# Performance work log

Measured on AMD Instinct MI355X. Metric: run time of the kernel, lower is better.

Reference implementation:

```python
import jax, jax.numpy as jnp
import numpy as np

WS = 8       # window size
NH = 6       # num heads
SHIFT = 4    # ws//2 since index=1 (shifted)
EPS = 1e-6


def _rel_pos_index(ws):
    coords = np.stack(np.meshgrid(np.arange(ws), np.arange(ws), indexing='ij'))  # (2,ws,ws)
    cf = coords.reshape(2, -1)
    rel = (cf[:, :, None] - cf[:, None, :]).transpose(1, 2, 0)  # (N,N,2)
    rel[..., 0] += ws - 1
    rel[..., 1] += ws - 1
    rel[..., 0] *= 2 * ws - 1
    return rel.sum(-1)  # (N,N) int


def _attn_mask(H, W, ws, shift):
    img = np.zeros((H, W))
    slices = (slice(0, -ws), slice(-ws, -shift), slice(-shift, None))
    cnt = 0
    for h in slices:
        for w in slices:
            img[h, w] = cnt
            cnt += 1
    mw = img.reshape(H // ws, ws, W // ws, ws).transpose(0, 2, 1, 3).reshape(-1, ws * ws)
    am = mw[:, None, :] - mw[:, :, None]  # (nW,N,N): unsqueeze(1) - unsqueeze(2)
    return np.where(am != 0, -100.0, 0.0).astype(np.float32)


def layernorm2d(x, w, b):
    mu = x.mean(1, keepdims=True)
    var = ((x - mu) ** 2).mean(1, keepdims=True)
    y = (x - mu) / jnp.sqrt(var + EPS)
    return w[None, :, None, None] * y + b[None, :, None, None]


def window_partition(x, ws):
    B, C, H, W = x.shape
    x = x.reshape(B, C, H // ws, ws, W // ws, ws)
    return x.transpose(0, 2, 4, 3, 5, 1).reshape(-1, ws * ws, C)


def window_reverse(win, ws, H, W):
    B = win.shape[0] // ((H // ws) * (W // ws))
    x = win.reshape(B, H // ws, W // ws, ws, ws, -1)
    return x.transpose(0, 5, 1, 3, 2, 4).reshape(B, -1, H, W)


def shifted_window_attn(x, qkv_w, qkv_b, proj_w, proj_b, rpb_table):
    B, C, H, W = x.shape
    N = WS * WS
    hd = C // NH
    scale = hd ** -0.5
    # faithful to original: raw reshape BCHW->BHWC (reinterpretation), roll, reshape back
    x = jnp.roll(x.reshape(B, H, W, C), (-SHIFT, -SHIFT), (1, 2)).reshape(B, C, H, W)
    win = window_partition(x, WS)  # (B_, N, C)
    B_ = win.shape[0]
    qkv = (win @ qkv_w + qkv_b).reshape(B_, N, 3, NH, hd).transpose(2, 0, 3, 1, 4)
    q, k, v = qkv[0] * scale, qkv[1], qkv[2]
    attn = jnp.einsum('bhnd,bhmd->bhnm', q, k)  # (B_,NH,N,N)
    rpi = _rel_pos_index(WS)
    bias = rpb_table[rpi.reshape(-1)].reshape(N, N, NH).transpose(2, 0, 1)
    attn = attn + bias[None]
    mask = jnp.asarray(_attn_mask(H, W, WS, SHIFT))  # (nW,N,N)
    nW = mask.shape[0]
    attn = attn.reshape(B_ // nW, nW, NH, N, N) + mask[None, :, None]
    attn = jax.nn.softmax(attn.reshape(B_, NH, N, N), axis=-1)
    out = jnp.einsum('bhnm,bhmd->bhnd', attn, v).transpose(0, 2, 1, 3).reshape(B_, N, C)
    out = out @ proj_w + proj_b
    return window_reverse(out, WS, H, W)


def channel_attention(y, ca_w, ca_b):
    gap = y.mean((2, 3))  # (B,C)
    s = jnp.einsum('bc,oc->bo', gap, ca_w) + ca_b  # 1x1 conv on pooled feature
    return s[:, :, None, None]


def mlp(y, fc1_w, fc1_b, fc2_w, fc2_b):
    B, C, H, W = y.shape
    t = y.transpose(0, 2, 3, 1)  # (B,H,W,C)
    t = jax.nn.gelu(t @ fc1_w + fc1_b, approximate=False)
    t = t @ fc2_w + fc2_b
    return t.transpose(0, 3, 1, 2)


def setup_inputs() -> dict:
    key = jax.random.key(0)
    ks = jax.random.split(key, 8)
    C, H, W, B = 192, 256, 256, 2
    hid = 2 * C
    sc = 0.02
    return {
        'x': jax.random.normal(ks[0], (B, C, H, W), jnp.float32),
        'norm1_w': jnp.ones((C,), jnp.float32),
        'norm1_b': jnp.zeros((C,), jnp.float32),
        'qkv_w': jax.random.normal(ks[1], (C, 3 * C), jnp.float32) * sc,
        'qkv_b': jnp.zeros((3 * C,), jnp.float32),
        'proj_w': jax.random.normal(ks[2], (C, C), jnp.float32) * sc,
        'proj_b': jnp.zeros((C,), jnp.float32),
        'rpb_table': jax.random.normal(ks[3], ((2 * WS - 1) ** 2, NH), jnp.float32) * sc,
        'ca_w': jax.random.normal(ks[4], (C, C), jnp.float32) * sc,
        'ca_b': jnp.zeros((C,), jnp.float32),
        'norm2_w': jnp.ones((C,), jnp.float32),
        'norm2_b': jnp.zeros((C,), jnp.float32),
        'fc1_w': jax.random.normal(ks[5], (C, hid), jnp.float32) * sc,
        'fc1_b': jnp.zeros((hid,), jnp.float32),
        'fc2_w': jax.random.normal(ks[6], (hid, C), jnp.float32) * sc,
        'fc2_b': jnp.zeros((C,), jnp.float32),
    }


def reference(x, norm1_w, norm1_b, qkv_w, qkv_b, proj_w, proj_b, rpb_table,
              ca_w, ca_b, norm2_w, norm2_b, fc1_w, fc1_b, fc2_w, fc2_b):
    y = layernorm2d(x, norm1_w, norm1_b)
    y = shifted_window_attn(y, qkv_w, qkv_b, proj_w, proj_b, rpb_table)
    y = y * channel_attention(y, ca_w, ca_b)
    x = x + y
    y2 = mlp(layernorm2d(x, norm2_w, norm2_b), fc1_w, fc1_b, fc2_w, fc2_b)
    return x + y2
```

## Files before the change

kernel.cpp:

```cpp
#include <hip/hip_runtime.h>
#include <hip/hip_bf16.h>
#include <stdint.h>

#define C_   192
#define H_   256
#define W_   256
#define HW_  65536
#define CHW  12582912
#define NH_  6
#define HID_ 384

typedef __attribute__((ext_vector_type(8))) __bf16 bf16x8;
typedef __attribute__((ext_vector_type(4))) float  fx4;

__device__ __forceinline__ uint16_t f2bf(float f) {
  uint32_t u = __builtin_bit_cast(uint32_t, f);
  u += 0x7fffu + ((u >> 16) & 1u);
  return (uint16_t)(u >> 16);
}
__device__ __forceinline__ float bf2f(uint16_t h) {
  uint32_t u = ((uint32_t)h) << 16;
  return __builtin_bit_cast(float, u);
}
__device__ __forceinline__ uint32_t pk2(float a, float b) {
  return (uint32_t)f2bf(a) | ((uint32_t)f2bf(b) << 16);
}
__device__ __forceinline__ bf16x8 ld8(const uint16_t* p) {
  uint4 v = *reinterpret_cast<const uint4*>(p);
  return __builtin_bit_cast(bf16x8, v);
}
__device__ __forceinline__ fx4 mfma16(bf16x8 a, bf16x8 b, fx4 c) {
  return __builtin_amdgcn_mfma_f32_16x16x32_bf16(a, b, c, 0, 0, 0);
}

__global__ __launch_bounds__(256) void prep_kernel(
    const float* __restrict__ qkv_w, const float* __restrict__ proj_w,
    const float* __restrict__ fc1_w, const float* __restrict__ fc2_w,
    const float* __restrict__ rpb,
    uint16_t* __restrict__ qkv_wt, uint16_t* __restrict__ proj_wt,
    uint16_t* __restrict__ fc1_wt, uint16_t* __restrict__ fc2_wt,
    float* __restrict__ rpbb) {
  int tid = blockIdx.x * 256 + threadIdx.x;
  if (tid < 576 * 192) {
    int f = tid / 192, k = tid % 192;
    qkv_wt[tid] = f2bf(qkv_w[k * 576 + f]);
  }
  int t1 = tid - 576 * 192;
  if (t1 >= 0 && t1 < 192 * 192) {
    int f = t1 / 192, k = t1 % 192;
    proj_wt[t1] = f2bf(proj_w[k * 192 + f]);
  }
  int t2 = t1 - 192 * 192;
  if (t2 >= 0 && t2 < 384 * 192) {
    int f = t2 / 192, k = t2 % 192;
    fc1_wt[t2] = f2bf(fc1_w[k * 384 + f]);
  }
  int t3 = t2 - 384 * 192;
  if (t3 >= 0 && t3 < 192 * 384) {
    int f = t3 / 384, k = t3 % 384;
    fc2_wt[t3] = f2bf(fc2_w[k * 192 + f]);
  }
  int t4 = t3 - 192 * 384;
  if (t4 >= 0 && t4 < 6 * 64 * 64) {
    int h = t4 / 4096, nm = t4 % 4096, n = nm / 64, m = nm % 64;
    int yn = n >> 3, xn = n & 7, ym = m >> 3, xm = m & 7;
    int idx = (yn - ym + 7) * 15 + (xn - xm + 7);
    rpbb[t4] = rpb[idx * NH_ + h];
  }
}

__global__ __launch_bounds__(256) void ln1_stats(const float* __restrict__ x,
                                                 float* __restrict__ mu,
                                                 float* __restrict__ rsig) {
  int t = blockIdx.x * 256 + threadIdx.x;
  int b = t >> 16, hw = t & 65535;
  const float* xp = x + (size_t)b * CHW + hw;
  float s = 0.f, sq = 0.f;
#pragma unroll 8
  for (int c = 0; c < C_; c++) {
    float v = xp[(size_t)c * HW_];
    s += v; sq += v * v;
  }
  float m = s * (1.0f / C_);
  float var = sq * (1.0f / C_) - m * m;
  mu[t] = m;
  rsig[t] = rsqrtf(var + 1e-6f);
}

__global__ __launch_bounds__(256) void ln1_apply_kernel(
    const float* __restrict__ x, const float* __restrict__ mu, const float* __restrict__ rsig,
    const float* __restrict__ n1w, const float* __restrict__ n1b,
    uint16_t* __restrict__ y_tok) {
  __shared__ __attribute__((aligned(16))) uint16_t tile[192 * 66];
  int wg = blockIdx.x;
  int b = wg >> 10, hw0 = (wg & 1023) << 6;
  int t = threadIdx.x;
  const float* xb = x + (size_t)b * CHW;
  const float* mub = mu + b * HW_;
  const float* rsb = rsig + b * HW_;
#pragma unroll 4
  for (int it = 0; it < 48; it++) {
    int id = it * 256 + t;
    int ca = id >> 6, pp = id & 63;
    int g = ca * 65536 + hw0 + pp;
    int h2 = g / 49152;
    int r = g - h2 * 49152;
    int w2 = r / 192;
    int c2 = r - w2 * 192;
    int f = ((h2 + 4) & 255) * 49152 + ((w2 + 4) & 255) * 192 + c2;
    int cnat = f >> 16;
    int hwn = f & 65535;
    float v = (xb[f] - mub[hwn]) * rsb[hwn] * n1w[cnat] + n1b[cnat];
    tile[ca * 66 + pp] = f2bf(v);
  }
  __syncthreads();
  uint16_t* yb = y_tok + ((size_t)(b * HW_ + hw0)) * C_;
#pragma unroll 4
  for (int it = 0; it < 48; it++) {
    int id = it * 256 + t;
    int pp = id / 192, ca = id - pp * 192;
    yb[id] = tile[ca * 66 + pp];
  }
}

__global__ __launch_bounds__(256, 2) void attn_kernel(
    const uint16_t* __restrict__ y_tok, const uint16_t* __restrict__ qkv_wt,
    const float* __restrict__ qkv_b, const uint16_t* __restrict__ proj_wt,
    const float* __restrict__ proj_b, const float* __restrict__ rpbb,
    uint16_t* __restrict__ y_attn, float* __restrict__ part) {
  __shared__ __attribute__((aligned(16))) uint16_t Qs[64 * 200];
  __shared__ __attribute__((aligned(16))) uint16_t Ks[64 * 200];
  __shared__ __attribute__((aligned(16))) uint16_t VT[32 * 72];
  __shared__ __attribute__((aligned(16))) uint16_t Ps[64 * 72];
  const int wg = blockIdx.x;
  const int b = wg >> 10, wid = wg & 1023;
  const int wh = wid >> 5, ww = wid & 31;
  const int t = threadIdx.x;
  const int w = t >> 6, l = t & 63;
  const int lane16 = l & 15, quad = l >> 4;
  const int trow = w * 16 + quad * 4;

  bf16x8 afr[4][6];
#pragma unroll
  for (int m = 0; m < 4; m++) {
    const int tok = m * 16 + lane16;
    const uint16_t* ap = y_tok +
        ((size_t)(b * HW_ + (wh * 8 + (tok >> 3)) * W_ + ww * 8 + (tok & 7))) * C_ + quad * 8;
#pragma unroll
    for (int k = 0; k < 6; k++) afr[m][k] = ld8(ap + k * 32);
  }

  const float scale = 0.17677669529663687f;
  uint32_t vpack[3][4][2];

#pragma unroll
  for (int j = 0; j < 3; j++) {
    const int nt = w + 4 * j;
    const uint16_t* bp = qkv_wt + (nt * 16 + lane16) * C_ + quad * 8;
    bf16x8 bfr[6];
#pragma unroll
    for (int k = 0; k < 6; k++) bfr[k] = ld8(bp + k * 32);
    fx4 acc[4];
#pragma unroll
    for (int m = 0; m < 4; m++) acc[m] = fx4{0.f, 0.f, 0.f, 0.f};
#pragma unroll
    for (int k = 0; k < 6; k++)
#pragma unroll
      for (int m = 0; m < 4; m++) acc[m] = mfma16(afr[m][k], bfr[k], acc[m]);
    const int f = nt * 16 + lane16;
    const float bias = qkv_b[f];
#pragma unroll
    for (int m = 0; m < 4; m++)
#pragma unroll
      for (int r = 0; r < 4; r++)
        Qs[(m * 16 + quad * 4 + r) * 200 + f] = f2bf((acc[m][r] + bias) * scale);
  }
#pragma unroll
  for (int j = 3; j < 6; j++) {
    const int nt = w + 4 * j;
    const uint16_t* bp = qkv_wt + (nt * 16 + lane16) * C_ + quad * 8;
    bf16x8 bfr[6];
#pragma unroll
    for (int k = 0; k < 6; k++) bfr[k] = ld8(bp + k * 32);
    fx4 acc[4];
#pragma unroll
    for (int m = 0; m < 4; m++) acc[m] = fx4{0.f, 0.f, 0.f, 0.f};
#pragma unroll
    for (int k = 0; k < 6; k++)
#pragma unroll
      for (int m = 0; m < 4; m++) acc[m] = mfma16(afr[m][k], bfr[k], acc[m]);
    const int f = nt * 16 + lane16;
    const float bias = qkv_b[f];
#pragma unroll
    for (int m = 0; m < 4; m++)
#pragma unroll
      for (int r = 0; r < 4; r++)
        Ks[(m * 16 + quad * 4 + r) * 200 + (f - 192)] = f2bf(acc[m][r] + bias);
  }
#pragma unroll
  for (int j = 6; j < 9; j++) {
    const int nt = w + 4 * j;
    const uint16_t* bp = qkv_wt + (nt * 16 + lane16) * C_ + quad * 8;
    bf16x8 bfr[6];
#pragma unroll
    for (int k = 0; k < 6; k++) bfr[k] = ld8(bp + k * 32);
    fx4 acc[4];
#pragma unroll
    for (int m = 0; m < 4; m++) acc[m] = fx4{0.f, 0.f, 0.f, 0.f};
#pragma unroll
    for (int k = 0; k < 6; k++)
#pragma unroll
      for (int m = 0; m < 4; m++) acc[m] = mfma16(afr[m][k], bfr[k], acc[m]);
    const float bias = qkv_b[nt * 16 + lane16];
    const int jv = j - 6;
#pragma unroll
    for (int m = 0; m < 4; m++) {
      vpack[jv][m][0] = pk2(acc[m][0] + bias, acc[m][1] + bias);
      vpack[jv][m][1] = pk2(acc[m][2] + bias, acc[m][3] + bias);
    }
  }

  const bool whe = (wh == 31), wwe = (ww == 31);

  for (int h = 0; h < 6; h++) {
    __syncthreads();
    {
      const int vt0 = 2 * h, vt1 = 2 * h + 1;
      if (w == (vt0 & 3)) {
        const int jv = vt0 >> 2;
#pragma unroll
        for (int m = 0; m < 4; m++) {
          uint2 vv; vv.x = vpack[jv][m][0]; vv.y = vpack[jv][m][1];
          *reinterpret_cast<uint2*>(&VT[lane16 * 72 + m * 16 + quad * 4]) = vv;
        }
      }
      if (w == (vt1 & 3)) {
        const int jv = vt1 >> 2;
#pragma unroll
        for (int m = 0; m < 4; m++) {
          uint2 vv; vv.x = vpack[jv][m][0]; vv.y = vpack[jv][m][1];
          *reinterpret_cast<uint2*>(&VT[(16 + lane16) * 72 + m * 16 + quad * 4]) = vv;
        }
      }
    }
    __syncthreads();

    const bf16x8 qa = ld8(&Qs[(w * 16 + lane16) * 200 + h * 32 + quad * 8]);
    fx4 sacc[4];
#pragma unroll
    for (int nt = 0; nt < 4; nt++) {
      const bf16x8 kb = ld8(&Ks[(nt * 16 + lane16) * 200 + h * 32 + quad * 8]);
      fx4 z = {0.f, 0.f, 0.f, 0.f};
      sacc[nt] = mfma16(qa, kb, z);
    }
    const float* rb = rpbb + h * 4096;
#pragma unroll
    for (int nt = 0; nt < 4; nt++) {
      const int ct = nt * 16 + lane16;
      const bool rbc = whe && ((ct >> 3) >= 4);
      const bool cbc = wwe && ((ct & 7) >= 4);
#pragma unroll
      for (int r = 0; r < 4; r++) {
        const int rt = trow + r;
        const bool rbr = whe && ((rt >> 3) >= 4);
        const bool cbr = wwe && ((rt & 7) >= 4);
        float v = sacc[nt][r] + rb[rt * 64 + ct];
        if (rbr != rbc || cbr != cbc) v -= 100.f;
        sacc[nt][r] = v;
      }
    }
    float sm[4];
#pragma unroll
    for (int r = 0; r < 4; r++) {
      float m = fmaxf(fmaxf(sacc[0][r], sacc[1][r]), fmaxf(sacc[2][r], sacc[3][r]));
      m = fmaxf(m, __shfl_xor(m, 1));
      m = fmaxf(m, __shfl_xor(m, 2));
      m = fmaxf(m, __shfl_xor(m, 4));
      m = fmaxf(m, __shfl_xor(m, 8));
      float s0 = 0.f;
#pragma unroll
      for (int nt = 0; nt < 4; nt++) {
        float e = exp2f((sacc[nt][r] - m) * 1.4426950408889634f);
        sacc[nt][r] = e; s0 += e;
      }
      s0 += __shfl_xor(s0, 1);
      s0 += __shfl_xor(s0, 2);
      s0 += __shfl_xor(s0, 4);
      s0 += __shfl_xor(s0, 8);
      sm[r] = s0;
    }
#pragma unroll
    for (int nt = 0; nt < 4; nt++)
#pragma unroll
      for (int r = 0; r < 4; r++)
        Ps[(trow + r) * 72 + nt * 16 + lane16] = f2bf(sacc[nt][r]);
    fx4 o0 = {0.f, 0.f, 0.f, 0.f}, o1 = {0.f, 0.f, 0.f, 0.f};
#pragma unroll
    for (int ks2 = 0; ks2 < 2; ks2++) {
      const bf16x8 pa = ld8(&Ps[(w * 16 + lane16) * 72 + ks2 * 32 + quad * 8]);
      const bf16x8 v0 = ld8(&VT[(lane16) * 72 + ks2 * 32 + quad * 8]);
      const bf16x8 v1 = ld8(&VT[(16 + lane16) * 72 + ks2 * 32 + quad * 8]);
      o0 = mfma16(pa, v0, o0);
      o1 = mfma16(pa, v1, o1);
    }
#pragma unroll
    for (int r = 0; r < 4; r++) {
      const float inv = 1.0f / sm[r];
      Qs[(trow + r) * 200 + h * 32 + lane16] = f2bf(o0[r] * inv);
      Qs[(trow + r) * 200 + h * 32 + 16 + lane16] = f2bf(o1[r] * inv);
    }
  }
  __syncthreads();

  bf16x8 ofr[4][6];
#pragma unroll
  for (int m = 0; m < 4; m++)
#pragma unroll
    for (int k = 0; k < 6; k++)
      ofr[m][k] = ld8(&Qs[(m * 16 + lane16) * 200 + k * 32 + quad * 8]);

  uint16_t* yb = y_attn + (size_t)b * HW_ * C_;
  uint32_t obase[4][4];
#pragma unroll
  for (int m = 0; m < 4; m++)
#pragma unroll
    for (int r = 0; r < 4; r++) {
      const int tok = m * 16 + quad * 4 + r;
      obase[m][r] = (uint32_t)(((wh * 8 + (tok >> 3)) * W_ + ww * 8 + (tok & 7)) * C_);
    }
#pragma unroll
  for (int j = 0; j < 3; j++) {
    const int nt = w + 4 * j;
    const uint16_t* bp = proj_wt + (nt * 16 + lane16) * C_ + quad * 8;
    bf16x8 bfr[6];
#pragma unroll
    for (int k = 0; k < 6; k++) bfr[k] = ld8(bp + k * 32);
    fx4 acc[4];
#pragma unroll
    for (int m = 0; m < 4; m++) acc[m] = fx4{0.f, 0.f, 0.f, 0.f};
#pragma unroll
    for (int k = 0; k < 6; k++)
#pragma unroll
      for (int m = 0; m < 4; m++) acc[m] = mfma16(ofr[m][k], bfr[k], acc[m]);
    const float pb = proj_b[nt * 16 + lane16];
    float cs = 0.f;
#pragma unroll
    for (int m = 0; m < 4; m++)
#pragma unroll
      for (int r = 0; r < 4; r++) {
        const float v = acc[m][r] + pb;
        yb[obase[m][r] + nt * 16 + lane16] = f2bf(v);
        cs += v;
      }
    cs += __shfl_xor(cs, 16);
    cs += __shfl_xor(cs, 32);
    if (l < 16) part[(size_t)wg * 192 + nt * 16 + lane16] = cs;
  }
}

__global__ __launch_bounds__(768) void ca_s_kernel(const float* __restrict__ part,
                                                   const float* __restrict__ ca_w,
                                                   const float* __restrict__ ca_b,
                                                   float* __restrict__ sbuf) {
  int b = blockIdx.x;
  int t = threadIdx.x;
  __shared__ float red[768];
  __shared__ float gap[192];
  int g = t / 192, c = t - g * 192;
  float s = 0.f;
#pragma unroll 8
  for (int i = g; i < 1024; i += 4) s += part[((size_t)b * 1024 + i) * 192 + c];
  red[t] = s;
  __syncthreads();
  if (t < 192)
    gap[t] = (red[t] + red[t + 192] + red[t + 384] + red[t + 576]) * (1.0f / 65536.0f);
  __syncthreads();
  if (t < 192) {
    float acc = ca_b[t];
#pragma unroll 8
    for (int c2 = 0; c2 < 192; c2++) acc += gap[c2] * ca_w[t * 192 + c2];
    sbuf[b * 192 + t] = acc;
  }
}

__global__ __launch_bounds__(256, 3) void resid_ln2(
    const float* __restrict__ x, const uint16_t* __restrict__ y_attn,
    const float* __restrict__ sbuf, const float* __restrict__ n2w,
    const float* __restrict__ n2b, uint16_t* __restrict__ t2) {
  __shared__ __attribute__((aligned(16))) float tile[192 * 66];
  __shared__ float red[512];
  __shared__ float mus[128];
  int wg = blockIdx.x;
  int b = wg >> 10, hw0 = (wg & 1023) << 6;
  int t = threadIdx.x;
#pragma unroll 4
  for (int it = 0; it < 48; it++) {
    int id = it * 256 + t;
    int c = id >> 6, p = id & 63;
    tile[c * 66 + p] = x[(size_t)b * CHW + (size_t)c * HW_ + hw0 + p];
  }
  __syncthreads();
#pragma unroll 4
  for (int it = 0; it < 48; it++) {
    int id = it * 256 + t;
    int p = id / 192, c = id - p * 192;
    float y = bf2f(y_attn[((size_t)(b * HW_ + hw0 + p)) * C_ + c]);
    tile[c * 66 + p] += sbuf[b * 192 + c] * y;
  }
  __syncthreads();
  {
    int p = t & 63, g = t >> 6;
    float s = 0.f, sq = 0.f;
    for (int c = g * 48; c < g * 48 + 48; c++) {
      float v = tile[c * 66 + p];
      s += v; sq += v * v;
    }
    red[g * 64 + p] = s;
    red[256 + g * 64 + p] = sq;
  }
  __syncthreads();
  if (t < 64) {
    float ss = red[t] + red[64 + t] + red[128 + t] + red[192 + t];
    float qq = red[256 + t] + red[320 + t] + red[384 + t] + red[448 + t];
    float m = ss * (1.0f / C_);
    float var = qq * (1.0f / C_) - m * m;
    mus[t] = m;
    mus[64 + t] = rsqrtf(var + 1e-6f);
  }
  __syncthreads();
#pragma unroll 4
  for (int it = 0; it < 48; it++) {
    int id = it * 256 + t;
    int p = id / 192, c = id - p * 192;
    float v = (tile[c * 66 + p] - mus[p]) * mus[64 + p] * n2w[c] + n2b[c];
    t2[((size_t)(b * HW_ + hw0 + p)) * C_ + c] = f2bf(v);
  }
}

__global__ __launch_bounds__(256, 3) void mlp_kernel(
    const uint16_t* __restrict__ t2, const uint16_t* __restrict__ fc1_wt,
    const float* __restrict__ fc1_b, const uint16_t* __restrict__ fc2_wt,
    const float* __restrict__ fc2_b, const float* __restrict__ x,
    const uint16_t* __restrict__ y_attn, const float* __restrict__ sbuf,
    float* __restrict__ out) {
  __shared__ __attribute__((aligned(16))) char smem[192 * 66 * 4];
  __shared__ float sarr[192];
  uint16_t* hbuf = (uint16_t*)smem;
  float* ftile = (float*)smem;
  int wg = blockIdx.x;
  int b = wg >> 10, hw0 = (wg & 1023) << 6;
  int t = threadIdx.x;
  int w = t >> 6, l = t & 63;
  int lane16 = l & 15, quad = l >> 4;
  if (t < 192) sarr[t] = sbuf[b * 192 + t];

  bf16x8 afr[4][6];
  const uint16_t* ab = t2 + ((size_t)(b * HW_ + hw0)) * C_;
#pragma unroll
  for (int m = 0; m < 4; m++) {
    const uint16_t* ap = ab + (m * 16 + lane16) * C_ + quad * 8;
#pragma unroll
    for (int k = 0; k < 6; k++) afr[m][k] = ld8(ap + k * 32);
  }

#pragma unroll
  for (int j = 0; j < 6; j++) {
    const int nt = w + 4 * j;
    const uint16_t* bp = fc1_wt + (nt * 16 + lane16) * C_ + quad * 8;
    bf16x8 bfr[6];
#pragma unroll
    for (int k = 0; k < 6; k++) bfr[k] = ld8(bp + k * 32);
    fx4 acc[4];
#pragma unroll
    for (int m = 0; m < 4; m++) acc[m] = fx4{0.f, 0.f, 0.f, 0.f};
#pragma unroll
    for (int k = 0; k < 6; k++)
#pragma unroll
      for (int m = 0; m < 4; m++) acc[m] = mfma16(afr[m][k], bfr[k], acc[m]);
    const float bias = fc1_b[nt * 16 + lane16];
#pragma unroll
    for (int m = 0; m < 4; m++)
#pragma unroll
      for (int r = 0; r < 4; r++) {
        float v = acc[m][r] + bias;
        float ge = 0.5f * v * (1.0f + erff(v * 0.7071067811865476f));
        hbuf[(m * 16 + quad * 4 + r) * 392 + nt * 16 + lane16] = f2bf(ge);
      }
  }
  __syncthreads();

  fx4 acc2[3][4];
#pragma unroll
  for (int j = 0; j < 3; j++)
#pragma unroll
    for (int m = 0; m < 4; m++) acc2[j][m] = fx4{0.f, 0.f, 0.f, 0.f};
#pragma unroll
  for (int kc = 0; kc < 4; kc++) {
    bf16x8 ha[4][3];
#pragma unroll
    for (int m = 0; m < 4; m++)
#pragma unroll
      for (int kk = 0; kk < 3; kk++)
        ha[m][kk] = ld8(&hbuf[(m * 16 + lane16) * 392 + kc * 96 + kk * 32 + quad * 8]);
#pragma unroll
    for (int j = 0; j < 3; j++) {
      const int nt = w + 4 * j;
      const uint16_t* bp = fc2_wt + (nt * 16 + lane16) * HID_ + kc * 96 + quad * 8;
#pragma unroll
      for (int kk = 0; kk < 3; kk++) {
        const bf16x8 bb = ld8(bp + kk * 32);
#pragma unroll
        for (int m = 0; m < 4; m++) acc2[j][m] = mfma16(ha[m][kk], bb, acc2[j][m]);
      }
    }
  }
  __syncthreads();

#pragma unroll
  for (int j = 0; j < 3; j++) {
    const int nt = w + 4 * j;
    const float bias = fc2_b[nt * 16 + lane16];
#pragma unroll
    for (int m = 0; m < 4; m++) {
      float* fp = &ftile[(nt * 16 + lane16) * 66 + m * 16 + quad * 4];
      float2 a = {acc2[j][m][0] + bias, acc2[j][m][1] + bias};
      float2 b2 = {acc2[j][m][2] + bias, acc2[j][m][3] + bias};
      *reinterpret_cast<float2*>(fp) = a;
      *reinterpret_cast<float2*>(fp + 2) = b2;
    }
  }
  __syncthreads();
#pragma unroll 4
  for (int it = 0; it < 48; it++) {
    int id = it * 256 + t;
    int p = id / 192, c = id - p * 192;
    float y = bf2f(y_attn[((size_t)(b * HW_ + hw0 + p)) * C_ + c]);
    ftile[c * 66 + p] += sarr[c] * y;
  }
  __syncthreads();
#pragma unroll 4
  for (int it = 0; it < 48; it++) {
    int id = it * 256 + t;
    int c = id >> 6, p = id & 63;
    size_t gi = (size_t)b * CHW + (size_t)c * HW_ + hw0 + p;
    out[gi] = x[gi] + ftile[c * 66 + p];
  }
}

extern "C" void kernel_launch(void* const* d_in, const int* in_sizes, int n_in,
                              void* d_out, int out_size, void* d_ws, size_t ws_size,
                              hipStream_t stream) {
  const float* x      = (const float*)d_in[0];
  const float* n1w    = (const float*)d_in[1];
  const float* n1b    = (const float*)d_in[2];
  const float* qkv_w  = (const float*)d_in[3];
  const float* qkv_b  = (const float*)d_in[4];
  const float* proj_w = (const float*)d_in[5];
  const float* proj_b = (const float*)d_in[6];
  const float* rpb    = (const float*)d_in[7];
  const float* ca_w   = (const float*)d_in[8];
  const float* ca_b   = (const float*)d_in[9];
  const float* n2w    = (const float*)d_in[10];
  const float* n2b    = (const float*)d_in[11];
  const float* fc1_w  = (const float*)d_in[12];
  const float* fc1_b  = (const float*)d_in[13];
  const float* fc2_w  = (const float*)d_in[14];
  const float* fc2_b  = (const float*)d_in[15];
  float* out = (float*)d_out;

  char* ws = (char*)d_ws;
  uint16_t* y_tok   = (uint16_t*)(ws + 0);
  uint16_t* y_attn  = (uint16_t*)(ws + 50331648);
  uint16_t* t2      = y_tok;
  float*    mu      = (float*)   (ws + 100663296);
  float*    rsig    = (float*)   (ws + 101187584);
  uint16_t* qkv_wt  = (uint16_t*)(ws + 101711872);
  uint16_t* proj_wt = (uint16_t*)(ws + 101933056);
  uint16_t* fc1_wt  = (uint16_t*)(ws + 102006784);
  uint16_t* fc2_wt  = (uint16_t*)(ws + 102154240);
  float*    rpbb    = (float*)   (ws + 102301696);
  float*    part    = (float*)   (ws + 102400000);
  float*    sbuf    = (float*)   (ws + 103972864);

  hipLaunchKernelGGL(prep_kernel, dim3(1248), dim3(256), 0, stream,
                     qkv_w, proj_w, fc1_w, fc2_w, rpb, qkv_wt, proj_wt, fc1_wt, fc2_wt, rpbb);
  hipLaunchKernelGGL(ln1_stats, dim3(512), dim3(256), 0, stream, x, mu, rsig);
  hipLaunchKernelGGL(ln1_apply_kernel, dim3(2048), dim3(256), 0, stream,
                     x, mu, rsig, n1w, n1b, y_tok);
  hipLaunchKernelGGL(attn_kernel, dim3(2048), dim3(256), 0, stream,
                     y_tok, qkv_wt, qkv_b, proj_wt, proj_b, rpbb, y_attn, part);
  hipLaunchKernelGGL(ca_s_kernel, dim3(2), dim3(768), 0, stream, part, ca_w, ca_b, sbuf);
  hipLaunchKernelGGL(resid_ln2, dim3(2048), dim3(256), 0, stream,
                     x, y_attn, sbuf, n2w, n2b, t2);
  hipLaunchKernelGGL(mlp_kernel, dim3(2048), dim3(256), 0, stream,
                     t2, fc1_wt, fc1_b, fc2_wt, fc2_b, x, y_attn, sbuf, out);
}
```

Before: 577.5 us.

## Shrink MLP tile to 32 tokens, use tanh GELU, split channel-attention reduction

The MLP kernel now handles 32 tokens per block instead of 64, launches twice as many blocks and raises the occupancy hint from 3 to 4. Each wave computes one 16-row M tile across a wider N range, which lowers register and LDS use per block. The erf GELU is replaced with an exp2/rcp tanh approximation, and the epilogue uses vectorized bf16x8 and float2 loads and stores. The channel-attention global pooling, previously done by 2 blocks, is split into a 128-block partial-sum kernel plus a small final kernel. In exchange, weight fragments are reused across fewer tokens, and the tanh GELU slightly changes numerics.

```diff
diff --git a/kernel.cpp b/kernel.cpp
--- a/kernel.cpp
+++ b/kernel.cpp
@@ -11,6 +11,7 @@
 #define HID_ 384
 
 typedef __attribute__((ext_vector_type(8))) __bf16 bf16x8;
+typedef __attribute__((ext_vector_type(8))) uint16_t u16x8;
 typedef __attribute__((ext_vector_type(4))) float  fx4;
 
 __device__ __forceinline__ uint16_t f2bf(float f) {
@@ -31,6 +32,14 @@
 }
 __device__ __forceinline__ fx4 mfma16(bf16x8 a, bf16x8 b, fx4 c) {
   return __builtin_amdgcn_mfma_f32_16x16x32_bf16(a, b, c, 0, 0, 0);
+}
+__device__ __forceinline__ float gelu_f(float v) {
+  float c2 = v * v;
+  float u = __builtin_fmaf(c2, 0.044715f, 1.0f) * v;
+  float e = exp2f(u * 2.3022084f);
+  float th = 1.0f - 2.0f * __builtin_amdgcn_rcpf(1.0f + e);
+  float hv = 0.5f * v;
+  return __builtin_fmaf(hv, th, hv);
 }
 
 __global__ __launch_bounds__(256) void prep_kernel(
@@ -358,29 +367,34 @@
   }
 }
 
-__global__ __launch_bounds__(768) void ca_s_kernel(const float* __restrict__ part,
-                                                   const float* __restrict__ ca_w,
-                                                   const float* __restrict__ ca_b,
-                                                   float* __restrict__ sbuf) {
+__global__ __launch_bounds__(192) void ca_gap(const float* __restrict__ part,
+                                              float* __restrict__ gpart) {
+  int blk = blockIdx.x;
+  int b = blk >> 6, ch = blk & 63;
+  int c = threadIdx.x;
+  float s = 0.f;
+#pragma unroll
+  for (int i = 0; i < 16; i++)
+    s += part[((size_t)b * 1024 + ch * 16 + i) * 192 + c];
+  gpart[blk * 192 + c] = s;
+}
+
+__global__ __launch_bounds__(192) void ca_s2(const float* __restrict__ gpart,
+                                             const float* __restrict__ ca_w,
+                                             const float* __restrict__ ca_b,
+                                             float* __restrict__ sbuf) {
   int b = blockIdx.x;
   int t = threadIdx.x;
-  __shared__ float red[768];
   __shared__ float gap[192];
-  int g = t / 192, c = t - g * 192;
   float s = 0.f;
 #pragma unroll 8
-  for (int i = g; i < 1024; i += 4) s += part[((size_t)b * 1024 + i) * 192 + c];
-  red[t] = s;
-  __syncthreads();
-  if (t < 192)
-    gap[t] = (red[t] + red[t + 192] + red[t + 384] + red[t + 576]) * (1.0f / 65536.0f);
-  __syncthreads();
-  if (t < 192) {
-    float acc = ca_b[t];
+  for (int i = 0; i < 64; i++) s += gpart[(b * 64 + i) * 192 + t];
+  gap[t] = s * (1.0f / 65536.0f);
+  __syncthreads();
+  float acc = ca_b[t];
 #pragma unroll 8
-    for (int c2 = 0; c2 < 192; c2++) acc += gap[c2] * ca_w[t * 192 + c2];
-    sbuf[b * 192 + t] = acc;
-  }
+  for (int c2 = 0; c2 < 192; c2++) acc += gap[c2] * ca_w[t * 192 + c2];
+  sbuf[b * 192 + t] = acc;
 }
 
 __global__ __launch_bounds__(256, 3) void resid_ln2(
@@ -437,113 +451,106 @@
   }
 }
 
-__global__ __launch_bounds__(256, 3) void mlp_kernel(
+__global__ __launch_bounds__(256, 4) void mlp_kernel(
     const uint16_t* __restrict__ t2, const uint16_t* __restrict__ fc1_wt,
     const float* __restrict__ fc1_b, const uint16_t* __restrict__ fc2_wt,
     const float* __restrict__ fc2_b, const float* __restrict__ x,
     const uint16_t* __restrict__ y_attn, const float* __restrict__ sbuf,
     float* __restrict__ out) {
-  __shared__ __attribute__((aligned(16))) char smem[192 * 66 * 4];
+  __shared__ __attribute__((aligned(16))) char smem[192 * 34 * 4];
   __shared__ float sarr[192];
   uint16_t* hbuf = (uint16_t*)smem;
   float* ftile = (float*)smem;
   int wg = blockIdx.x;
-  int b = wg >> 10, hw0 = (wg & 1023) << 6;
+  int b = wg >> 11, hw0 = (wg & 2047) << 5;
   int t = threadIdx.x;
   int w = t >> 6, l = t & 63;
   int lane16 = l & 15, quad = l >> 4;
+  const int m1 = w & 1, ng = w >> 1;
   if (t < 192) sarr[t] = sbuf[b * 192 + t];
 
-  bf16x8 afr[4][6];
-  const uint16_t* ab = t2 + ((size_t)(b * HW_ + hw0)) * C_;
-#pragma unroll
-  for (int m = 0; m < 4; m++) {
-    const uint16_t* ap = ab + (m * 16 + lane16) * C_ + quad * 8;
-#pragma unroll
-    for (int k = 0; k < 6; k++) afr[m][k] = ld8(ap + k * 32);
-  }
-
-#pragma unroll
-  for (int j = 0; j < 6; j++) {
-    const int nt = w + 4 * j;
+  bf16x8 afr[6];
+  {
+    const uint16_t* ap = t2 + ((size_t)(b * HW_ + hw0 + m1 * 16 + lane16)) * C_ + quad * 8;
+#pragma unroll
+    for (int k = 0; k < 6; k++) afr[k] = ld8(ap + k * 32);
+  }
+
+#pragma unroll 4
+  for (int j = 0; j < 12; j++) {
+    const int nt = ng * 12 + j;
     const uint16_t* bp = fc1_wt + (nt * 16 + lane16) * C_ + quad * 8;
     bf16x8 bfr[6];
 #pragma unroll
     for (int k = 0; k < 6; k++) bfr[k] = ld8(bp + k * 32);
-    fx4 acc[4];
-#pragma unroll
-    for (int m = 0; m < 4; m++) acc[m] = fx4{0.f, 0.f, 0.f, 0.f};
-#pragma unroll
-    for (int k = 0; k < 6; k++)
-#pragma unroll
-      for (int m = 0; m < 4; m++) acc[m] = mfma16(afr[m][k], bfr[k], acc[m]);
+    fx4 acc = {0.f, 0.f, 0.f, 0.f};
+#pragma unroll
+    for (int k = 0; k < 6; k++) acc = mfma16(afr[k], bfr[k], acc);
     const float bias = fc1_b[nt * 16 + lane16];
 #pragma unroll
-    for (int m = 0; m < 4; m++)
-#pragma unroll
-      for (int r = 0; r < 4; r++) {
-        float v = acc[m][r] + bias;
-        float ge = 0.5f * v * (1.0f + erff(v * 0.7071067811865476f));
-        hbuf[(m * 16 + quad * 4 + r) * 392 + nt * 16 + lane16] = f2bf(ge);
+    for (int r = 0; r < 4; r++) {
+      float ge = gelu_f(acc[r] + bias);
+      hbuf[(m1 * 16 + quad * 4 + r) * 392 + nt * 16 + lane16] = f2bf(ge);
+    }
+  }
+  __syncthreads();
+
+  fx4 acc2[6];
+#pragma unroll
+  for (int j = 0; j < 6; j++) acc2[j] = fx4{0.f, 0.f, 0.f, 0.f};
+#pragma unroll
+  for (int kc = 0; kc < 4; kc++) {
+#pragma unroll
+    for (int kk = 0; kk < 3; kk++) {
+      const bf16x8 ha = ld8(&hbuf[(m1 * 16 + lane16) * 392 + kc * 96 + kk * 32 + quad * 8]);
+#pragma unroll
+      for (int j = 0; j < 6; j++) {
+        const int nt2 = ng * 6 + j;
+        const bf16x8 bb = ld8(fc2_wt + (nt2 * 16 + lane16) * HID_ + kc * 96 + kk * 32 + quad * 8);
+        acc2[j] = mfma16(ha, bb, acc2[j]);
       }
-  }
-  __syncthreads();
-
-  fx4 acc2[3][4];
-#pragma unroll
-  for (int j = 0; j < 3; j++)
-#pragma unroll
-    for (int m = 0; m < 4; m++) acc2[j][m] = fx4{0.f, 0.f, 0.f, 0.f};
-#pragma unroll
-  for (int kc = 0; kc < 4; kc++) {
-    bf16x8 ha[4][3];
-#pragma unroll
-    for (int m = 0; m < 4; m++)
-#pragma unroll
-      for (int kk = 0; kk < 3; kk++)
-        ha[m][kk] = ld8(&hbuf[(m * 16 + lane16) * 392 + kc * 96 + kk * 32 + quad * 8]);
-#pragma unroll
-    for (int j = 0; j < 3; j++) {
-      const int nt = w + 4 * j;
-      const uint16_t* bp = fc2_wt + (nt * 16 + lane16) * HID_ + kc * 96 + quad * 8;
-#pragma unroll
-      for (int kk = 0; kk < 3; kk++) {
-        const bf16x8 bb = ld8(bp + kk * 32);
-#pragma unroll
-        for (int m = 0; m < 4; m++) acc2[j][m] = mfma16(ha[m][kk], bb, acc2[j][m]);
+    }
+  }
+  __syncthreads();
+
+#pragma unroll
+  for (int j = 0; j < 6; j++) {
+    const int nt2 = ng * 6 + j;
+    const float bias = fc2_b[nt2 * 16 + lane16];
+    float* fp = &ftile[(nt2 * 16 + lane16) * 34 + m1 * 16 + quad * 4];
+    float2 aa = {acc2[j][0] + bias, acc2[j][1] + bias};
+    float2 bb2 = {acc2[j][2] + bias, acc2[j][3] + bias};
+    *reinterpret_cast<float2*>(fp) = aa;
+    *reinterpret_cast<float2*>(fp + 2) = bb2;
+  }
+  __syncthreads();
+
+  {
+    const int p = t & 31, q = t >> 5;
+    const uint16_t* yr = y_attn + ((size_t)(b * HW_ + hw0 + p)) * C_;
+#pragma unroll
+    for (int i = 0; i < 3; i++) {
+      int qq = q * 3 + i;
+      u16x8 uv = __builtin_bit_cast(u16x8, ld8(yr + qq * 8));
+#pragma unroll
+      for (int j = 0; j < 8; j++) {
+        int c = qq * 8 + j;
+        ftile[c * 34 + p] += sarr[c] * bf2f(uv[j]);
       }
     }
   }
   __syncthreads();
 
-#pragma unroll
-  for (int j = 0; j < 3; j++) {
-    const int nt = w + 4 * j;
-    const float bias = fc2_b[nt * 16 + lane16];
-#pragma unroll
-    for (int m = 0; m < 4; m++) {
-      float* fp = &ftile[(nt * 16 + lane16) * 66 + m * 16 + quad * 4];
-      float2 a = {acc2[j][m][0] + bias, acc2[j][m][1] + bias};
-      float2 b2 = {acc2[j][m][2] + bias, acc2[j][m][3] + bias};
-      *reinterpret_cast<float2*>(fp) = a;
-      *reinterpret_cast<float2*>(fp + 2) = b2;
-    }
-  }
-  __syncthreads();
-#pragma unroll 4
-  for (int it = 0; it < 48; it++) {
-    int id = it * 256 + t;
-    int p = id / 192, c = id - p * 192;
-    float y = bf2f(y_attn[((size_t)(b * HW_ + hw0 + p)) * C_ + c]);
-    ftile[c * 66 + p] += sarr[c] * y;
-  }
-  __syncthreads();
-#pragma unroll 4
-  for (int it = 0; it < 48; it++) {
-    int id = it * 256 + t;
-    int c = id >> 6, p = id & 63;
-    size_t gi = (size_t)b * CHW + (size_t)c * HW_ + hw0 + p;
-    out[gi] = x[gi] + ftile[c * 66 + p];
+  const float* xb = x + (size_t)b * CHW + hw0;
+  float* ob = out + (size_t)b * CHW + hw0;
+#pragma unroll
+  for (int i = 0; i < 12; i++) {
+    int id = i * 256 + t;
+    int c = id >> 4, p2 = id & 15;
+    float2 xv = *reinterpret_cast<const float2*>(xb + (size_t)c * HW_ + p2 * 2);
+    float2 fv = *reinterpret_cast<const float2*>(&ftile[c * 34 + p2 * 2]);
+    float2 ov = {xv.x + fv.x, xv.y + fv.y};
+    *reinterpret_cast<float2*>(ob + (size_t)c * HW_ + p2 * 2) = ov;
   }
 }
 
@@ -581,6 +588,7 @@
   float*    rpbb    = (float*)   (ws + 102301696);
   float*    part    = (float*)   (ws + 102400000);
   float*    sbuf    = (float*)   (ws + 103972864);
+  float*    gpart   = (float*)   (ws + 103974400);
 
   hipLaunchKernelGGL(prep_kernel, dim3(1248), dim3(256), 0, stream,
                      qkv_w, proj_w, fc1_w, fc2_w, rpb, qkv_wt, proj_wt, fc1_wt, fc2_wt, rpbb);
@@ -589,9 +597,10 @@
                      x, mu, rsig, n1w, n1b, y_tok);
   hipLaunchKernelGGL(attn_kernel, dim3(2048), dim3(256), 0, stream,
                      y_tok, qkv_wt, qkv_b, proj_wt, proj_b, rpbb, y_attn, part);
-  hipLaunchKernelGGL(ca_s_kernel, dim3(2), dim3(768), 0, stream, part, ca_w, ca_b, sbuf);
+  hipLaunchKernelGGL(ca_gap, dim3(128), dim3(192), 0, stream, part, gpart);
+  hipLaunchKernelGGL(ca_s2, dim3(2), dim3(192), 0, stream, gpart, ca_w, ca_b, sbuf);
   hipLaunchKernelGGL(resid_ln2, dim3(2048), dim3(256), 0, stream,
                      x, y_attn, sbuf, n2w, n2b, t2);
-  hipLaunchKernelGGL(mlp_kernel, dim3(2048), dim3(256), 0, stream,
+  hipLaunchKernelGGL(mlp_kernel, dim3(4096), dim3(256), 0, stream,
                      t2, fc1_wt, fc1_b, fc2_wt, fc2_b, x, y_attn, sbuf, out);
 }
```

Measured after the change: 685.3 us. 18.7% more time.
